# Optimization experiments

Measured on AMD Instinct MI355X. Metric: run time of the kernel, lower is better.

## Reference

```python
import jax, jax.numpy as jnp
import numpy as np

N_NODES = 50000
N_EDGES = 800000
IN_DIM = 128
HID = 128
OUT_DIM = 2


def setup_inputs() -> dict:
    key = jax.random.key(0)
    ks = jax.random.split(key, 10)
    s_in = 1.0 / np.sqrt(IN_DIM)
    s_cat = 1.0 / np.sqrt(2 * HID)
    s_h = 1.0 / np.sqrt(HID)
    return {
        "x": jax.random.normal(ks[0], (N_NODES, IN_DIM), dtype=jnp.float32),
        "edge_index": jax.random.randint(ks[1], (2, N_EDGES), 0, N_NODES, dtype=jnp.int64),
        "W_in": jax.random.uniform(ks[2], (IN_DIM, HID), jnp.float32, -s_in, s_in),
        "b_in": jnp.zeros((HID,), jnp.float32),
        "W1": jax.random.uniform(ks[3], (2 * HID, HID), jnp.float32, -s_cat, s_cat),
        "b1": jnp.zeros((HID,), jnp.float32),
        "W2": jax.random.uniform(ks[4], (HID, HID), jnp.float32, -s_h, s_h),
        "b2": jnp.zeros((HID,), jnp.float32),
        "Wc": jax.random.uniform(ks[5], (HID, OUT_DIM), jnp.float32, -s_h, s_h),
        "bc": jnp.zeros((OUT_DIM,), jnp.float32),
    }


def reference(x, edge_index, W_in, b_in, W1, b1, W2, b2, Wc, bc):
    # Input projection (eval mode: dropout is identity)
    h = jax.nn.relu(x @ W_in + b_in)                      # [N, H]
    src, dst = edge_index[0], edge_index[1]               # PyG: x_j = x[src], x_i = x[dst]
    # Per-edge message: MLP(h_i || h_j). Split the first Linear over the concat
    # halves to avoid materializing the [E, 2H] concat buffer.
    m = h[dst] @ W1[:HID] + h[src] @ W1[HID:] + b1        # [E, H]
    m = jax.nn.relu(m) @ W2 + b2                          # [E, H]
    # Scatter-add aggregation into destination nodes
    h2 = jax.ops.segment_sum(m, dst, num_segments=N_NODES)  # [N, H]
    h2 = jax.nn.relu(h2)
    return h2 @ Wc + bc                                   # [N, OUT]
```

## Files before the change

### kernel.cpp

```cpp
#include <hip/hip_runtime.h>
#include <hip/hip_bf16.h>

#define N_NODES 50000
#define N_EDGES 800000
#define HID 128
#define NPROJ 391
#define CAP 48
#define OVF_MAX 8192
#define NBIN 196
#define BINSH 8
#define BINCAP 5120
#define NCOARSE 98

typedef __bf16 bf16x8 __attribute__((ext_vector_type(8)));
typedef float f32x4 __attribute__((ext_vector_type(4)));

__global__ __launch_bounds__(256) void prep_kernel(
    const float* __restrict__ Win, const float* __restrict__ W1,
    const float* __restrict__ W2, __bf16* __restrict__ Wsw,
    int* __restrict__ curz)
{
    int id = blockIdx.x * 256 + threadIdx.x;
    int m     = id >> 14;
    int rem   = id & 16383;
    int j     = rem & 7;
    int lane  = (rem >> 3) & 63;
    int ntile = (rem >> 9) & 7;
    int kstep = rem >> 12;
    int k = kstep * 32 + (lane >> 4) * 8 + j;
    int n = ntile * 16 + (lane & 15);
    float v;
    if (m == 0)      v = Win[k * HID + n];
    else if (m == 1) v = W1[k * HID + n];
    else if (m == 2) v = W1[(k + HID) * HID + n];
    else             v = W2[k * HID + n];
    Wsw[id] = (__bf16)v;
    if (id < N_NODES + NBIN + 1) curz[id] = 0;
}

__global__ __launch_bounds__(256) void coarse_kernel(
    const int* __restrict__ eidx, int* __restrict__ bincnt,
    unsigned int* __restrict__ binbuf, int* __restrict__ cursor,
    int* __restrict__ ovf_cnt, uint2* __restrict__ ovf)
{
    __shared__ int lcnt[NBIN];
    __shared__ int lbase[NBIN];
    int tid = threadIdx.x;
    int e0 = blockIdx.x * 8192;
    for (int i = tid; i < NBIN; i += 256) lcnt[i] = 0;
    __syncthreads();
    for (int k = 0; k < 32; ++k) {
        int e = e0 + k * 256 + tid;
        if (e < N_EDGES)
            atomicAdd(&lcnt[eidx[N_EDGES + e] >> BINSH], 1);
    }
    __syncthreads();
    for (int i = tid; i < NBIN; i += 256) {
        lbase[i] = atomicAdd(&bincnt[i], lcnt[i]);
        lcnt[i] = 0;
    }
    __syncthreads();
    for (int k = 0; k < 32; ++k) {
        int e = e0 + k * 256 + tid;
        if (e < N_EDGES) {
            int d = eidx[N_EDGES + e];
            int s = eidx[e];
            int b = d >> BINSH;
            int p = lbase[b] + atomicAdd(&lcnt[b], 1);
            if (p < BINCAP) {
                binbuf[b * BINCAP + p] = ((unsigned)d << 16) | (unsigned)s;
            } else {
                int o = atomicAdd(ovf_cnt, 1);
                if (o < OVF_MAX) ovf[o] = make_uint2((unsigned)d, (unsigned)s);
                atomicAdd(&cursor[d], 1);
            }
        }
    }
}

__global__ __launch_bounds__(256) void fine_kernel(
    const int* __restrict__ bincnt, const unsigned int* __restrict__ binbuf,
    unsigned short* __restrict__ srt, int* __restrict__ cursor,
    int* __restrict__ ovf_cnt, uint2* __restrict__ ovf)
{
    __shared__ int lcur[256];
    int tid = threadIdx.x;
    int bin = blockIdx.x;
    lcur[tid] = 0;
    __syncthreads();
    int n = bincnt[bin];
    if (n > BINCAP) n = BINCAP;
    const unsigned int* src = binbuf + bin * BINCAP;

#define SCAT(U) do {                                                   \
        unsigned int u_ = (U);                                         \
        int d_ = (int)(u_ >> 16);                                      \
        int p_ = atomicAdd(&lcur[d_ & 255], 1);                        \
        if (p_ < CAP) srt[d_ * CAP + p_] = (unsigned short)(u_ & 0xffffu); \
        else { int o_ = atomicAdd(ovf_cnt, 1);                         \
               if (o_ < OVF_MAX) ovf[o_] = make_uint2((unsigned)d_, u_ & 0xffffu); } \
    } while (0)

    int i = tid;
    for (; i + 768 < n; i += 1024) {
        unsigned int u0 = src[i];
        unsigned int u1 = src[i + 256];
        unsigned int u2 = src[i + 512];
        unsigned int u3 = src[i + 768];
        SCAT(u0); SCAT(u1); SCAT(u2); SCAT(u3);
    }
    for (; i < n; i += 256) SCAT(src[i]);
#undef SCAT

    __syncthreads();
    int node = (bin << BINSH) + tid;
    if (node < N_NODES)
        cursor[node] += lcur[tid];
}

__global__ __launch_bounds__(256) void projp_kernel(
    const float* __restrict__ x, const __bf16* __restrict__ Wsw,
    const float* __restrict__ b_in, const float* __restrict__ b1,
    float* __restrict__ P1a, __bf16* __restrict__ P1b)
{
    int bb = blockIdx.x;
    int tid = threadIdx.x;

    __shared__ __bf16 At[128][136];
    int wave = tid >> 6, lane = tid & 63;
    int r_lane = lane & 15, quad = lane >> 4;
    int m0 = bb * 128;

    for (int i = tid; i < 128 * 32; i += 256) {
        int r = i >> 5, c = i & 31;
        int row = m0 + r;
        float4 v = make_float4(0.f, 0.f, 0.f, 0.f);
        if (row < N_NODES) v = *(const float4*)(x + (long)row * HID + c * 4);
        __bf16* dst = &At[r][c * 4];
        dst[0] = (__bf16)v.x; dst[1] = (__bf16)v.y;
        dst[2] = (__bf16)v.z; dst[3] = (__bf16)v.w;
    }
    __syncthreads();

    {
        f32x4 acc[2][8] = {};
#pragma unroll
        for (int ks = 0; ks < 4; ++ks) {
            int kb = ks * 32 + quad * 8;
            bf16x8 bf[8];
#pragma unroll
            for (int n = 0; n < 8; ++n)
                bf[n] = *(const bf16x8*)(Wsw + ((ks * 8 + n) * 64 + lane) * 8);
            bf16x8 a0 = *(const bf16x8*)(&At[wave * 32 + r_lane][kb]);
            bf16x8 a1 = *(const bf16x8*)(&At[wave * 32 + 16 + r_lane][kb]);
#pragma unroll
            for (int n = 0; n < 8; ++n) {
                acc[0][n] = __builtin_amdgcn_mfma_f32_16x16x32_bf16(a0, bf[n], acc[0][n], 0, 0, 0);
                acc[1][n] = __builtin_amdgcn_mfma_f32_16x16x32_bf16(a1, bf[n], acc[1][n], 0, 0, 0);
            }
        }
#pragma unroll
        for (int n = 0; n < 8; ++n) {
            int col = n * 16 + r_lane;
            float bias = b_in[col];
#pragma unroll
            for (int mt = 0; mt < 2; ++mt) {
                int rb = wave * 32 + mt * 16 + quad * 4;
#pragma unroll
                for (int r = 0; r < 4; ++r) {
                    float v = acc[mt][n][r] + bias;
                    At[rb + r][col] = (__bf16)(v > 0.f ? v : 0.f);
                }
            }
        }
    }
    __syncthreads();

    {
        const __bf16* W1a = Wsw + 16384;
        f32x4 acc[2][8] = {};
#pragma unroll
        for (int ks = 0; ks < 4; ++ks) {
            int kb = ks * 32 + quad * 8;
            bf16x8 bf[8];
#pragma unroll
            for (int n = 0; n < 8; ++n)
                bf[n] = *(const bf16x8*)(W1a + ((ks * 8 + n) * 64 + lane) * 8);
            bf16x8 a0 = *(const bf16x8*)(&At[wave * 32 + r_lane][kb]);
            bf16x8 a1 = *(const bf16x8*)(&At[wave * 32 + 16 + r_lane][kb]);
#pragma unroll
            for (int n = 0; n < 8; ++n) {
                acc[0][n] = __builtin_amdgcn_mfma_f32_16x16x32_bf16(a0, bf[n], acc[0][n], 0, 0, 0);
                acc[1][n] = __builtin_amdgcn_mfma_f32_16x16x32_bf16(a1, bf[n], acc[1][n], 0, 0, 0);
            }
        }
#pragma unroll
        for (int n = 0; n < 8; ++n) {
            int col = n * 16 + r_lane;
            float bias = b1[col];
#pragma unroll
            for (int mt = 0; mt < 2; ++mt) {
                int rbase = m0 + wave * 32 + mt * 16 + quad * 4;
#pragma unroll
                for (int r = 0; r < 4; ++r) {
                    int row = rbase + r;
                    if (row < N_NODES)
                        P1a[(long)row * HID + col] = acc[mt][n][r] + bias;
                }
            }
        }
    }

    {
        const __bf16* W1b = Wsw + 32768;
        f32x4 acc[2][8] = {};
#pragma unroll
        for (int ks = 0; ks < 4; ++ks) {
            int kb = ks * 32 + quad * 8;
            bf16x8 bf[8];
#pragma unroll
            for (int n = 0; n < 8; ++n)
                bf[n] = *(const bf16x8*)(W1b + ((ks * 8 + n) * 64 + lane) * 8);
            bf16x8 a0 = *(const bf16x8*)(&At[wave * 32 + r_lane][kb]);
            bf16x8 a1 = *(const bf16x8*)(&At[wave * 32 + 16 + r_lane][kb]);
#pragma unroll
            for (int n = 0; n < 8; ++n) {
                acc[0][n] = __builtin_amdgcn_mfma_f32_16x16x32_bf16(a0, bf[n], acc[0][n], 0, 0, 0);
                acc[1][n] = __builtin_amdgcn_mfma_f32_16x16x32_bf16(a1, bf[n], acc[1][n], 0, 0, 0);
            }
        }
#pragma unroll
        for (int n = 0; n < 8; ++n) {
            int col = n * 16 + r_lane;
#pragma unroll
            for (int mt = 0; mt < 2; ++mt) {
                int rbase = m0 + wave * 32 + mt * 16 + quad * 4;
#pragma unroll
                for (int r = 0; r < 4; ++r) {
                    int row = rbase + r;
                    if (row < N_NODES)
                        P1b[(long)row * HID + col] = (__bf16)acc[mt][n][r];
                }
            }
        }
    }
}

__device__ inline void acc8(float4& rA, float4& rB,
                            const float4 paA, const float4 paB, uint4 q)
{
    float t;
    t = paA.x + __uint_as_float(q.x << 16);         rA.x += t > 0.f ? t : 0.f;
    t = paA.y + __uint_as_float(q.x & 0xffff0000u); rA.y += t > 0.f ? t : 0.f;
    t = paA.z + __uint_as_float(q.y << 16);         rA.z += t > 0.f ? t : 0.f;
    t = paA.w + __uint_as_float(q.y & 0xffff0000u); rA.w += t > 0.f ? t : 0.f;
    t = paB.x + __uint_as_float(q.z << 16);         rB.x += t > 0.f ? t : 0.f;
    t = paB.y + __uint_as_float(q.z & 0xffff0000u); rB.y += t > 0.f ? t : 0.f;
    t = paB.z + __uint_as_float(q.w << 16);         rB.z += t > 0.f ? t : 0.f;
    t = paB.w + __uint_as_float(q.w & 0xffff0000u); rB.w += t > 0.f ? t : 0.f;
}

__global__ __launch_bounds__(512) void aggnode_kernel(
    const float* __restrict__ P1a, const __bf16* __restrict__ P1b,
    const unsigned short* __restrict__ srt, const int* __restrict__ cursor,
    const int* __restrict__ ovf_cnt, const uint2* __restrict__ ovf,
    const __bf16* __restrict__ Wsw, const float* __restrict__ b2,
    const float* __restrict__ Wc, const float* __restrict__ bc,
    float* __restrict__ out)
{
    __shared__ __bf16 At[128][136];
    int tid = threadIdx.x;
    int m0 = blockIdx.x * 128;
    int oc = *ovf_cnt;
    if (oc > OVF_MAX) oc = OVF_MAX;

    {
        int team = tid >> 4;
        int tl = tid & 15;
        for (int g = 0; g < 4; ++g) {
            int r = team * 4 + g;
            int node = m0 + r;
            float4 rA = make_float4(0.f, 0.f, 0.f, 0.f);
            float4 rB = make_float4(0.f, 0.f, 0.f, 0.f);
            if (node < N_NODES) {
                int beg = node * CAP;
                int degT = cursor[node];
                int deg = degT > CAP ? CAP : degT;
                const float* par = P1a + (long)node * HID + tl * 8;
                float4 paA = *(const float4*)par;
                float4 paB = *(const float4*)(par + 4);
                int nb = deg >> 3;
                int j = nb << 3;
                if (nb) {
                    int s0 = srt[beg + 0];
                    int s1 = srt[beg + 1];
                    int s2 = srt[beg + 2];
                    int s3 = srt[beg + 3];
                    int s4 = srt[beg + 4];
                    int s5 = srt[beg + 5];
                    int s6 = srt[beg + 6];
                    int s7 = srt[beg + 7];
                    for (int b = 1; b < nb; ++b) {
                        uint4 q0 = *(const uint4*)(P1b + (long)s0 * HID + tl * 8);
                        uint4 q1 = *(const uint4*)(P1b + (long)s1 * HID + tl * 8);
                        uint4 q2 = *(const uint4*)(P1b + (long)s2 * HID + tl * 8);
                        uint4 q3 = *(const uint4*)(P1b + (long)s3 * HID + tl * 8);
                        uint4 q4 = *(const uint4*)(P1b + (long)s4 * HID + tl * 8);
                        uint4 q5 = *(const uint4*)(P1b + (long)s5 * HID + tl * 8);
                        uint4 q6 = *(const uint4*)(P1b + (long)s6 * HID + tl * 8);
                        uint4 q7 = *(const uint4*)(P1b + (long)s7 * HID + tl * 8);
                        int bb8 = beg + b * 8;
                        s0 = srt[bb8 + 0];
                        s1 = srt[bb8 + 1];
                        s2 = srt[bb8 + 2];
                        s3 = srt[bb8 + 3];
                        s4 = srt[bb8 + 4];
                        s5 = srt[bb8 + 5];
                        s6 = srt[bb8 + 6];
                        s7 = srt[bb8 + 7];
                        acc8(rA, rB, paA, paB, q0);
                        acc8(rA, rB, paA, paB, q1);
                        acc8(rA, rB, paA, paB, q2);
                        acc8(rA, rB, paA, paB, q3);
                        acc8(rA, rB, paA, paB, q4);
                        acc8(rA, rB, paA, paB, q5);
                        acc8(rA, rB, paA, paB, q6);
                        acc8(rA, rB, paA, paB, q7);
                    }
                    uint4 q0 = *(const uint4*)(P1b + (long)s0 * HID + tl * 8);
                    uint4 q1 = *(const uint4*)(P1b + (long)s1 * HID + tl * 8);
                    uint4 q2 = *(const uint4*)(P1b + (long)s2 * HID + tl * 8);
                    uint4 q3 = *(const uint4*)(P1b + (long)s3 * HID + tl * 8);
                    uint4 q4 = *(const uint4*)(P1b + (long)s4 * HID + tl * 8);
                    uint4 q5 = *(const uint4*)(P1b + (long)s5 * HID + tl * 8);
                    uint4 q6 = *(const uint4*)(P1b + (long)s6 * HID + tl * 8);
                    uint4 q7 = *(const uint4*)(P1b + (long)s7 * HID + tl * 8);
                    acc8(rA, rB, paA, paB, q0);
                    acc8(rA, rB, paA, paB, q1);
                    acc8(rA, rB, paA, paB, q2);
                    acc8(rA, rB, paA, paB, q3);
                    acc8(rA, rB, paA, paB, q4);
                    acc8(rA, rB, paA, paB, q5);
                    acc8(rA, rB, paA, paB, q6);
                    acc8(rA, rB, paA, paB, q7);
                }
                for (; j < deg; ++j) {
                    int s = srt[beg + j];
                    uint4 q = *(const uint4*)(P1b + (long)s * HID + tl * 8);
                    acc8(rA, rB, paA, paB, q);
                }
                if (oc) {
                    for (int t = 0; t < oc; ++t) {
                        uint2 e = ovf[t];
                        if ((int)e.x == node) {
                            uint4 q = *(const uint4*)(P1b + (long)e.y * HID + tl * 8);
                            acc8(rA, rB, paA, paB, q);
                        }
                    }
                }
            }
            __bf16 vv[8];
            vv[0] = (__bf16)rA.x; vv[1] = (__bf16)rA.y;
            vv[2] = (__bf16)rA.z; vv[3] = (__bf16)rA.w;
            vv[4] = (__bf16)rB.x; vv[5] = (__bf16)rB.y;
            vv[6] = (__bf16)rB.z; vv[7] = (__bf16)rB.w;
            *(uint4*)(&At[r][tl * 8]) = *(uint4*)vv;
        }
    }
    __syncthreads();

    int wave = tid >> 6, lane = tid & 63;
    int r_lane = lane & 15, quad = lane >> 4;
    const __bf16* W2f = Wsw + 49152;
    f32x4 acc[8] = {};
#pragma unroll
    for (int ks = 0; ks < 4; ++ks) {
        int kb = ks * 32 + quad * 8;
        bf16x8 bf[8];
#pragma unroll
        for (int n = 0; n < 8; ++n)
            bf[n] = *(const bf16x8*)(W2f + ((ks * 8 + n) * 64 + lane) * 8);
        bf16x8 a0 = *(const bf16x8*)(&At[wave * 16 + r_lane][kb]);
#pragma unroll
        for (int n = 0; n < 8; ++n)
            acc[n] = __builtin_amdgcn_mfma_f32_16x16x32_bf16(a0, bf[n], acc[n], 0, 0, 0);
    }

#pragma unroll
    for (int r = 0; r < 4; ++r) {
        int row = m0 + wave * 16 + quad * 4 + r;
        float deg = (row < N_NODES) ? (float)cursor[row] : 0.f;
        float s0 = 0.f, s1 = 0.f;
#pragma unroll
        for (int n = 0; n < 8; ++n) {
            int col = n * 16 + r_lane;
            float v = acc[n][r] + deg * b2[col];
            v = v > 0.f ? v : 0.f;
            s0 += v * Wc[col * 2 + 0];
            s1 += v * Wc[col * 2 + 1];
        }
#pragma unroll
        for (int off = 1; off < 16; off <<= 1) {
            s0 += __shfl_xor(s0, off);
            s1 += __shfl_xor(s1, off);
        }
        if (r_lane == 0 && row < N_NODES) {
            out[(long)row * 2 + 0] = s0 + bc[0];
            out[(long)row * 2 + 1] = s1 + bc[1];
        }
    }
}

extern "C" void kernel_launch(void* const* d_in, const int* in_sizes, int n_in,
                              void* d_out, int out_size, void* d_ws, size_t ws_size,
                              hipStream_t stream) {
    const float* x    = (const float*)d_in[0];
    const int* eidx   = (const int*)d_in[1];
    const float* W_in = (const float*)d_in[2];
    const float* b_in = (const float*)d_in[3];
    const float* W1   = (const float*)d_in[4];
    const float* b1   = (const float*)d_in[5];
    const float* W2   = (const float*)d_in[6];
    const float* b2   = (const float*)d_in[7];
    const float* Wc   = (const float*)d_in[8];
    const float* bc   = (const float*)d_in[9];
    float* out = (float*)d_out;

    char* ws = (char*)d_ws;
    float*  P1a  = (float*)(ws + 0);
    unsigned int* binbuf = (unsigned int*)(ws + 0);
    __bf16* P1b  = (__bf16*)(ws + 25600000);
    unsigned short* srt = (unsigned short*)(ws + 38400000);
    int* cursor  = (int*)(ws + 43200000);
    int* bincnt  = cursor + N_NODES;
    int* ovf_cnt = cursor + N_NODES + NBIN;
    uint2* ovf   = (uint2*)(ws + 43400800);
    __bf16* Wsw  = (__bf16*)(ws + 43466368);

    prep_kernel<<<256, 256, 0, stream>>>(W_in, W1, W2, Wsw, cursor);
    coarse_kernel<<<NCOARSE, 256, 0, stream>>>(eidx, bincnt, binbuf, cursor,
                                               ovf_cnt, ovf);
    fine_kernel<<<NBIN, 256, 0, stream>>>(bincnt, binbuf, srt, cursor,
                                          ovf_cnt, ovf);
    projp_kernel<<<NPROJ, 256, 0, stream>>>(x, Wsw, b_in, b1, P1a, P1b);
    aggnode_kernel<<<(N_NODES + 127) / 128, 512, 0, stream>>>(
        P1a, P1b, srt, cursor, ovf_cnt, ovf, Wsw, b2, Wc, bc, out);
}
```

Baseline: 191.0 us.

## Fuse edge binning with projection and do fine sort inside aggregation kernel

The coarse binning pass is merged into the projection kernel as extra blocks, so both run in one launch and can overlap. The separate fine-sort kernel is removed: each aggregation block scans its coarse bin and builds per-node neighbor lists in shared memory, with a small local overflow list. This removes a kernel launch and the global round trip through the sorted index array. In exchange, each bin is scanned twice and shared memory use rises, which may cut occupancy.

```diff
diff --git a/kernel.cpp b/kernel.cpp
--- a/kernel.cpp
+++ b/kernel.cpp
@@ -9,7 +9,7 @@
 #define OVF_MAX 8192
 #define NBIN 196
 #define BINSH 8
-#define BINCAP 5120
+#define BINCAP 4608
 #define NCOARSE 98
 
 typedef __bf16 bf16x8 __attribute__((ext_vector_type(8)));
@@ -38,95 +38,54 @@
     if (id < N_NODES + NBIN + 1) curz[id] = 0;
 }
 
-__global__ __launch_bounds__(256) void coarse_kernel(
+__global__ __launch_bounds__(256) void fused_kernel(
+    const float* __restrict__ x, const __bf16* __restrict__ Wsw,
+    const float* __restrict__ b_in, const float* __restrict__ b1,
+    float* __restrict__ P1a, __bf16* __restrict__ P1b,
     const int* __restrict__ eidx, int* __restrict__ bincnt,
     unsigned int* __restrict__ binbuf, int* __restrict__ cursor,
     int* __restrict__ ovf_cnt, uint2* __restrict__ ovf)
 {
-    __shared__ int lcnt[NBIN];
-    __shared__ int lbase[NBIN];
-    int tid = threadIdx.x;
-    int e0 = blockIdx.x * 8192;
-    for (int i = tid; i < NBIN; i += 256) lcnt[i] = 0;
-    __syncthreads();
-    for (int k = 0; k < 32; ++k) {
-        int e = e0 + k * 256 + tid;
-        if (e < N_EDGES)
-            atomicAdd(&lcnt[eidx[N_EDGES + e] >> BINSH], 1);
-    }
-    __syncthreads();
-    for (int i = tid; i < NBIN; i += 256) {
-        lbase[i] = atomicAdd(&bincnt[i], lcnt[i]);
-        lcnt[i] = 0;
-    }
-    __syncthreads();
-    for (int k = 0; k < 32; ++k) {
-        int e = e0 + k * 256 + tid;
-        if (e < N_EDGES) {
-            int d = eidx[N_EDGES + e];
-            int s = eidx[e];
-            int b = d >> BINSH;
-            int p = lbase[b] + atomicAdd(&lcnt[b], 1);
-            if (p < BINCAP) {
-                binbuf[b * BINCAP + p] = ((unsigned)d << 16) | (unsigned)s;
-            } else {
-                int o = atomicAdd(ovf_cnt, 1);
-                if (o < OVF_MAX) ovf[o] = make_uint2((unsigned)d, (unsigned)s);
-                atomicAdd(&cursor[d], 1);
-            }
-        }
-    }
-}
-
-__global__ __launch_bounds__(256) void fine_kernel(
-    const int* __restrict__ bincnt, const unsigned int* __restrict__ binbuf,
-    unsigned short* __restrict__ srt, int* __restrict__ cursor,
-    int* __restrict__ ovf_cnt, uint2* __restrict__ ovf)
-{
-    __shared__ int lcur[256];
-    int tid = threadIdx.x;
-    int bin = blockIdx.x;
-    lcur[tid] = 0;
-    __syncthreads();
-    int n = bincnt[bin];
-    if (n > BINCAP) n = BINCAP;
-    const unsigned int* src = binbuf + bin * BINCAP;
-
-#define SCAT(U) do {                                                   \
-        unsigned int u_ = (U);                                         \
-        int d_ = (int)(u_ >> 16);                                      \
-        int p_ = atomicAdd(&lcur[d_ & 255], 1);                        \
-        if (p_ < CAP) srt[d_ * CAP + p_] = (unsigned short)(u_ & 0xffffu); \
-        else { int o_ = atomicAdd(ovf_cnt, 1);                         \
-               if (o_ < OVF_MAX) ovf[o_] = make_uint2((unsigned)d_, u_ & 0xffffu); } \
-    } while (0)
-
-    int i = tid;
-    for (; i + 768 < n; i += 1024) {
-        unsigned int u0 = src[i];
-        unsigned int u1 = src[i + 256];
-        unsigned int u2 = src[i + 512];
-        unsigned int u3 = src[i + 768];
-        SCAT(u0); SCAT(u1); SCAT(u2); SCAT(u3);
-    }
-    for (; i < n; i += 256) SCAT(src[i]);
-#undef SCAT
-
-    __syncthreads();
-    int node = (bin << BINSH) + tid;
-    if (node < N_NODES)
-        cursor[node] += lcur[tid];
-}
-
-__global__ __launch_bounds__(256) void projp_kernel(
-    const float* __restrict__ x, const __bf16* __restrict__ Wsw,
-    const float* __restrict__ b_in, const float* __restrict__ b1,
-    float* __restrict__ P1a, __bf16* __restrict__ P1b)
-{
+    __shared__ __bf16 At[128][136];
     int bb = blockIdx.x;
     int tid = threadIdx.x;
 
-    __shared__ __bf16 At[128][136];
+    if (bb >= NPROJ) {
+        int* lcnt  = (int*)&At[0][0];
+        int* lbase = lcnt + NBIN;
+        int e0 = (bb - NPROJ) * 8192;
+        for (int i = tid; i < NBIN; i += 256) lcnt[i] = 0;
+        __syncthreads();
+        for (int k = 0; k < 32; ++k) {
+            int e = e0 + k * 256 + tid;
+            if (e < N_EDGES)
+                atomicAdd(&lcnt[eidx[N_EDGES + e] >> BINSH], 1);
+        }
+        __syncthreads();
+        for (int i = tid; i < NBIN; i += 256) {
+            lbase[i] = atomicAdd(&bincnt[i], lcnt[i]);
+            lcnt[i] = 0;
+        }
+        __syncthreads();
+        for (int k = 0; k < 32; ++k) {
+            int e = e0 + k * 256 + tid;
+            if (e < N_EDGES) {
+                int d = eidx[N_EDGES + e];
+                int s = eidx[e];
+                int b = d >> BINSH;
+                int p = lbase[b] + atomicAdd(&lcnt[b], 1);
+                if (p < BINCAP) {
+                    binbuf[b * BINCAP + p] = ((unsigned)d << 16) | (unsigned)s;
+                } else {
+                    int o = atomicAdd(ovf_cnt, 1);
+                    if (o < OVF_MAX) ovf[o] = make_uint2((unsigned)d, (unsigned)s);
+                    atomicAdd(&cursor[d], 1);
+                }
+            }
+        }
+        return;
+    }
+
     int wave = tid >> 6, lane = tid & 63;
     int r_lane = lane & 15, quad = lane >> 4;
     int m0 = bb * 128;
@@ -262,17 +221,51 @@
 
 __global__ __launch_bounds__(512) void aggnode_kernel(
     const float* __restrict__ P1a, const __bf16* __restrict__ P1b,
-    const unsigned short* __restrict__ srt, const int* __restrict__ cursor,
-    const int* __restrict__ ovf_cnt, const uint2* __restrict__ ovf,
-    const __bf16* __restrict__ Wsw, const float* __restrict__ b2,
-    const float* __restrict__ Wc, const float* __restrict__ bc,
-    float* __restrict__ out)
+    const unsigned int* __restrict__ binbuf, const int* __restrict__ bincnt,
+    const int* __restrict__ cursor, const int* __restrict__ ovf_cnt,
+    const uint2* __restrict__ ovf, const __bf16* __restrict__ Wsw,
+    const float* __restrict__ b2, const float* __restrict__ Wc,
+    const float* __restrict__ bc, float* __restrict__ out)
 {
     __shared__ __bf16 At[128][136];
+    __shared__ unsigned short idx[128][CAP];
+    __shared__ int lcur[128];
+    __shared__ int degS[128];
+    __shared__ unsigned int lovf[128];
+    __shared__ int lovf_cnt;
     int tid = threadIdx.x;
-    int m0 = blockIdx.x * 128;
+    int blk = blockIdx.x;
+    int m0 = blk * 128;
     int oc = *ovf_cnt;
     if (oc > OVF_MAX) oc = OVF_MAX;
+
+    if (tid < 128) lcur[tid] = 0;
+    if (tid == 0) lovf_cnt = 0;
+    __syncthreads();
+    {
+        int bin = blk >> 1;
+        int n = bincnt[bin];
+        if (n > BINCAP) n = BINCAP;
+        const unsigned int* src = binbuf + bin * BINCAP;
+        for (int i = tid; i < n; i += 512) {
+            unsigned int u = src[i];
+            int d = (int)(u >> 16);
+            if ((d >> 7) == blk) {
+                int p = atomicAdd(&lcur[d & 127], 1);
+                if (p < CAP) idx[d & 127][p] = (unsigned short)(u & 0xffffu);
+                else { int o = atomicAdd(&lovf_cnt, 1);
+                       if (o < 128) lovf[o] = u; }
+            }
+        }
+    }
+    __syncthreads();
+    if (tid < 128) {
+        int node = m0 + tid;
+        degS[tid] = lcur[tid] + ((node < N_NODES) ? cursor[node] : 0);
+    }
+    __syncthreads();
+    int lc = lovf_cnt;
+    if (lc > 128) lc = 128;
 
     {
         int team = tid >> 4;
@@ -283,50 +276,22 @@
             float4 rA = make_float4(0.f, 0.f, 0.f, 0.f);
             float4 rB = make_float4(0.f, 0.f, 0.f, 0.f);
             if (node < N_NODES) {
-                int beg = node * CAP;
-                int degT = cursor[node];
-                int deg = degT > CAP ? CAP : degT;
+                int deg = lcur[r];
+                if (deg > CAP) deg = CAP;
+                const unsigned short* ip = idx[r];
                 const float* par = P1a + (long)node * HID + tl * 8;
                 float4 paA = *(const float4*)par;
                 float4 paB = *(const float4*)(par + 4);
-                int nb = deg >> 3;
-                int j = nb << 3;
-                if (nb) {
-                    int s0 = srt[beg + 0];
-                    int s1 = srt[beg + 1];
-                    int s2 = srt[beg + 2];
-                    int s3 = srt[beg + 3];
-                    int s4 = srt[beg + 4];
-                    int s5 = srt[beg + 5];
-                    int s6 = srt[beg + 6];
-                    int s7 = srt[beg + 7];
-                    for (int b = 1; b < nb; ++b) {
-                        uint4 q0 = *(const uint4*)(P1b + (long)s0 * HID + tl * 8);
-                        uint4 q1 = *(const uint4*)(P1b + (long)s1 * HID + tl * 8);
-                        uint4 q2 = *(const uint4*)(P1b + (long)s2 * HID + tl * 8);
-                        uint4 q3 = *(const uint4*)(P1b + (long)s3 * HID + tl * 8);
-                        uint4 q4 = *(const uint4*)(P1b + (long)s4 * HID + tl * 8);
-                        uint4 q5 = *(const uint4*)(P1b + (long)s5 * HID + tl * 8);
-                        uint4 q6 = *(const uint4*)(P1b + (long)s6 * HID + tl * 8);
-                        uint4 q7 = *(const uint4*)(P1b + (long)s7 * HID + tl * 8);
-                        int bb8 = beg + b * 8;
-                        s0 = srt[bb8 + 0];
-                        s1 = srt[bb8 + 1];
-                        s2 = srt[bb8 + 2];
-                        s3 = srt[bb8 + 3];
-                        s4 = srt[bb8 + 4];
-                        s5 = srt[bb8 + 5];
-                        s6 = srt[bb8 + 6];
-                        s7 = srt[bb8 + 7];
-                        acc8(rA, rB, paA, paB, q0);
-                        acc8(rA, rB, paA, paB, q1);
-                        acc8(rA, rB, paA, paB, q2);
-                        acc8(rA, rB, paA, paB, q3);
-                        acc8(rA, rB, paA, paB, q4);
-                        acc8(rA, rB, paA, paB, q5);
-                        acc8(rA, rB, paA, paB, q6);
-                        acc8(rA, rB, paA, paB, q7);
-                    }
+                int j = 0;
+                for (; j + 8 <= deg; j += 8) {
+                    int s0 = ip[j + 0];
+                    int s1 = ip[j + 1];
+                    int s2 = ip[j + 2];
+                    int s3 = ip[j + 3];
+                    int s4 = ip[j + 4];
+                    int s5 = ip[j + 5];
+                    int s6 = ip[j + 6];
+                    int s7 = ip[j + 7];
                     uint4 q0 = *(const uint4*)(P1b + (long)s0 * HID + tl * 8);
                     uint4 q1 = *(const uint4*)(P1b + (long)s1 * HID + tl * 8);
                     uint4 q2 = *(const uint4*)(P1b + (long)s2 * HID + tl * 8);
@@ -345,9 +310,16 @@
                     acc8(rA, rB, paA, paB, q7);
                 }
                 for (; j < deg; ++j) {
-                    int s = srt[beg + j];
+                    int s = ip[j];
                     uint4 q = *(const uint4*)(P1b + (long)s * HID + tl * 8);
                     acc8(rA, rB, paA, paB, q);
+                }
+                for (int t = 0; t < lc; ++t) {
+                    unsigned int u = lovf[t];
+                    if ((int)(u >> 16) == node) {
+                        uint4 q = *(const uint4*)(P1b + (long)(u & 0xffffu) * HID + tl * 8);
+                        acc8(rA, rB, paA, paB, q);
+                    }
                 }
                 if (oc) {
                     for (int t = 0; t < oc; ++t) {
@@ -388,8 +360,9 @@
 
 #pragma unroll
     for (int r = 0; r < 4; ++r) {
-        int row = m0 + wave * 16 + quad * 4 + r;
-        float deg = (row < N_NODES) ? (float)cursor[row] : 0.f;
+        int lr = wave * 16 + quad * 4 + r;
+        int row = m0 + lr;
+        float deg = (float)degS[lr];
         float s0 = 0.f, s1 = 0.f;
 #pragma unroll
         for (int n = 0; n < 8; ++n) {
@@ -428,21 +401,17 @@
 
     char* ws = (char*)d_ws;
     float*  P1a  = (float*)(ws + 0);
-    unsigned int* binbuf = (unsigned int*)(ws + 0);
     __bf16* P1b  = (__bf16*)(ws + 25600000);
-    unsigned short* srt = (unsigned short*)(ws + 38400000);
-    int* cursor  = (int*)(ws + 43200000);
+    int* cursor  = (int*)(ws + 38400000);
     int* bincnt  = cursor + N_NODES;
     int* ovf_cnt = cursor + N_NODES + NBIN;
-    uint2* ovf   = (uint2*)(ws + 43400800);
-    __bf16* Wsw  = (__bf16*)(ws + 43466368);
+    uint2* ovf   = (uint2*)(ws + 38600800);
+    __bf16* Wsw  = (__bf16*)(ws + 38666368);
+    unsigned int* binbuf = (unsigned int*)(ws + 38797440);
 
     prep_kernel<<<256, 256, 0, stream>>>(W_in, W1, W2, Wsw, cursor);
-    coarse_kernel<<<NCOARSE, 256, 0, stream>>>(eidx, bincnt, binbuf, cursor,
-                                               ovf_cnt, ovf);
-    fine_kernel<<<NBIN, 256, 0, stream>>>(bincnt, binbuf, srt, cursor,
-                                          ovf_cnt, ovf);
-    projp_kernel<<<NPROJ, 256, 0, stream>>>(x, Wsw, b_in, b1, P1a, P1b);
+    fused_kernel<<<NPROJ + NCOARSE, 256, 0, stream>>>(
+        x, Wsw, b_in, b1, P1a, P1b, eidx, bincnt, binbuf, cursor, ovf_cnt, ovf);
     aggnode_kernel<<<(N_NODES + 127) / 128, 512, 0, stream>>>(
-        P1a, P1b, srt, cursor, ovf_cnt, ovf, Wsw, b2, Wc, bc, out);
+        P1a, P1b, binbuf, bincnt, cursor, ovf_cnt, ovf, Wsw, b2, Wc, bc, out);
 }
```

Result: faster. 160.5 us (-16.0%).
